# Kernel optimization log

Measured on AMD Instinct MI355X. Metric: run time of the kernel, lower is better.

## Reference

```python
import jax, jax.numpy as jnp
import numpy as np

B, L_IN, L_OUT, N, COV, EMB, H = 32, 336, 48, 512, 4, 32, 64
C = 1 + COV
D_IN = EMB + COV


def setup_inputs() -> dict:
    key = jax.random.key(0)
    ks = jax.random.split(key, 16)
    s = 1.0 / np.sqrt(H)

    def rn(k, shape, scale):
        return jax.random.normal(k, shape, jnp.float32) * scale

    return {
        "history_data": jax.random.normal(ks[0], (B, L_IN, N, C), jnp.float32),
        "future_data": jax.random.normal(ks[1], (B, L_OUT, N, C), jnp.float32),
        "emb_W": rn(ks[2], (EMB, 1), 0.5),
        "emb_b": rn(ks[3], (EMB,), 0.1),
        "W_ih0": rn(ks[4], (4 * H, D_IN), s),
        "W_hh0": rn(ks[5], (4 * H, H), s),
        "b_ih0": rn(ks[6], (4 * H,), s),
        "b_hh0": rn(ks[7], (4 * H,), s),
        "W_ih1": rn(ks[8], (4 * H, H), s),
        "W_hh1": rn(ks[9], (4 * H, H), s),
        "b_ih1": rn(ks[10], (4 * H,), s),
        "b_hh1": rn(ks[11], (4 * H,), s),
        "head_W": rn(ks[12], (2, H), s),
        "head_b": rn(ks[13], (2,), 0.1),
        "train": 1,
    }


def _lstm_cell(x_t, h, c, W_ih, W_hh, b_ih, b_hh):
    # gate order i, f, g, o (torch nn.LSTM convention)
    g = x_t @ W_ih.T + b_ih + h @ W_hh.T + b_hh
    i, f, gg, o = jnp.split(g, 4, axis=-1)
    c = jax.nn.sigmoid(f) * c + jax.nn.sigmoid(i) * jnp.tanh(gg)
    h = jax.nn.sigmoid(o) * jnp.tanh(c)
    return h, c


def _deepar_forward(history_data, future_data, emb_W, emb_b,
                    W_ih0, W_hh0, b_ih0, b_hh0,
                    W_ih1, W_hh1, b_ih1, b_hh1,
                    head_W, head_b):
    Bb, L_in, Nn, _ = history_data.shape
    L_out = future_data.shape[1]
    # [B, L_in+L_out, N, .]
    target = jnp.concatenate([history_data[..., 0:1], future_data[..., 0:1]], axis=1)
    covar = jnp.concatenate([history_data[..., 1:], future_data[..., 1:]], axis=1)
    # train=True branch: teacher forcing for t = 1 .. L-1
    prev = target[:, :-1]        # [B, T, N, 1]
    cov_t = covar[:, 1:]         # [B, T, N, COV]
    emb = prev @ emb_W.T + emb_b  # [B, T, N, EMB]
    x = jnp.concatenate([emb, cov_t], axis=-1)      # [B, T, N, EMB+COV]
    T = x.shape[1]
    x = x.transpose(1, 0, 2, 3).reshape(T, Bb * Nn, -1)  # scan over time
    Hh = W_hh0.shape[1]
    z = jnp.zeros((Bb * Nn, Hh), x.dtype)

    def step(carry, x_t):
        h0, c0, h1, c1 = carry
        h0, c0 = _lstm_cell(x_t, h0, c0, W_ih0, W_hh0, b_ih0, b_hh0)
        h1, c1 = _lstm_cell(h0, h1, c1, W_ih1, W_hh1, b_ih1, b_hh1)
        p = jax.nn.relu(h1) @ head_W.T + head_b       # [BN, 2]
        mu = p[:, 0:1]
        sigma = jax.nn.softplus(p[:, 1:2])
        return (h0, c0, h1, c1), jnp.concatenate([mu, sigma], axis=-1)

    _, outs = jax.lax.scan(step, (z, z, z, z), x)     # [T, BN, 2]
    outs = outs.reshape(T, Bb, Nn, 2).transpose(1, 0, 2, 3)  # [B, T, N, 2]
    return outs[:, -L_out:]


def reference(history_data, future_data, emb_W, emb_b,
              W_ih0, W_hh0, b_ih0, b_hh0,
              W_ih1, W_hh1, b_ih1, b_hh1,
              head_W, head_b, train):
    # train is a static Python int (1 = teacher forcing branch implemented here)
    return _deepar_forward(history_data, future_data, emb_W, emb_b,
                           W_ih0, W_hh0, b_ih0, b_hh0,
                           W_ih1, W_hh1, b_ih1, b_hh1,
                           head_W, head_b)
```

## Files before the change

kernel.cpp:

```cpp
#include <hip/hip_runtime.h>


#define T_STEPS 383
#define AST 168

typedef __attribute__((ext_vector_type(8))) short short8;
typedef __attribute__((ext_vector_type(4))) short s16x4;
typedef __attribute__((ext_vector_type(4))) float floatx4;

__device__ __forceinline__ unsigned short f2bf(float f){
  union { float f; unsigned u; } v; v.f = f;
  unsigned u = v.u + 0x7fffu + ((v.u >> 16) & 1u);
  return (unsigned short)(u >> 16);
}
__device__ __forceinline__ unsigned short f2bf_fast(float f){
  union { float f; unsigned u; } v; v.f = f;
  return (unsigned short)((v.u + 0x8000u) >> 16);
}
__device__ __forceinline__ float bf2f(unsigned short b){
  union { unsigned u; float f; } v; v.u = ((unsigned)b) << 16; return v.f;
}
__device__ __forceinline__ float fsig(float x){
  return __builtin_amdgcn_rcpf(1.f + __expf(-x));
}
__device__ __forceinline__ float ftanh(float x){
  return 1.f - 2.f * __builtin_amdgcn_rcpf(1.f + __expf(2.f * x));
}

__global__ __launch_bounds__(512, 4) void deepar_kernel(
    const float* __restrict__ hist, const float* __restrict__ fut,
    const float* __restrict__ embW, const float* __restrict__ embB,
    const float* __restrict__ Wih0, const float* __restrict__ Whh0,
    const float* __restrict__ bih0, const float* __restrict__ bhh0,
    const float* __restrict__ Wih1, const float* __restrict__ Whh1,
    const float* __restrict__ bih1, const float* __restrict__ bhh1,
    const float* __restrict__ headW, const float* __restrict__ headB,
    float* __restrict__ outp)
{
  const int tid  = threadIdx.x;
  const int lane = tid & 63;
  const int wv   = tid >> 6;
  const int l15  = lane & 15;
  const int quad = lane >> 4;
  const int koff = quad * 8;
  const int jt   = wv >> 1;
  const int mt   = wv & 1;
  const int srow = mt * 16 + l15;
  const int jbase = jt * 16 + quad * 4;

  const int b  = blockIdx.x >> 4;
  const int n0 = (blockIdx.x & 15) * 32;

  __shared__ __align__(16) unsigned short A[32 * AST];
  __shared__ __align__(16) unsigned short W1[64 * 64 * 8];
  __shared__ float HW[128];

  for (int i = tid; i < 32 * AST; i += 512) A[i] = 0;
  if (tid < 128) HW[tid] = headW[tid];
  __syncthreads();
  if (tid < 32){
    A[tid * AST + 133] = 0x3f80;
    A[tid * AST + 134] = 0x3f80;
  }
  const float hb0 = headB[0], hb1 = headB[1];

  short8 bf0[4][3];
  floatx4 bi1v[4];
  #pragma unroll
  for (int g = 0; g < 4; ++g){
    const int rf = g * 64 + jt * 16 + l15;
    float u = 0.f, bb = bih0[rf] + bhh0[rf];
    #pragma unroll
    for (int e = 0; e < 32; ++e){
      float wval = Wih0[rf * 36 + e];
      u  += wval * embW[e];
      bb += wval * embB[e];
    }
    const unsigned short bbq = f2bf(bb);
    const float bbr = bb - bf2f(bbq);
    #pragma unroll
    for (int kf = 0; kf < 2; ++kf)
      #pragma unroll
      for (int j = 0; j < 8; ++j)
        bf0[g][kf][j] = (short)f2bf(Whh0[rf * 64 + kf * 32 + koff + j]);
    #pragma unroll
    for (int j = 0; j < 8; ++j){
      const int kk = koff + j;
      float v = 0.f;
      if (kk == 0) v = u;
      else if (kk >= 1 && kk <= 4) v = Wih0[rf * 36 + 32 + (kk - 1)];
      else if (kk == 6) v = bbr;
      unsigned short q16 = (kk == 5) ? bbq : f2bf(v);
      bf0[g][2][j] = (short)q16;
    }
    #pragma unroll
    for (int q = 0; q < 4; ++q){
      const int re = g * 64 + jt * 16 + quad * 4 + q;
      bi1v[g][q] = bih1[re] + bhh1[re];
    }
    if (mt == 0){
      #pragma unroll
      for (int kf = 0; kf < 4; ++kf){
        const float* src = (kf < 2) ? (Wih1 + rf * 64 + kf * 32)
                                    : (Whh1 + rf * 64 + (kf - 2) * 32);
        short8 w;
        #pragma unroll
        for (int j = 0; j < 8; ++j)
          w[j] = (short)f2bf(src[koff + j]);
        *(short8*)&W1[((jt * 16 + g * 4 + kf) * 64 + lane) * 8] = w;
      }
    }
  }

  const bool isPrev = (tid < 32);
  const bool isCov  = (tid >= 64 && tid < 192);
  int ss = 0, cc = 0;
  if (isPrev){ ss = tid; cc = 0; }
  if (isCov) { ss = (tid - 64) >> 2; cc = 1 + ((tid - 64) & 3); }
  const int myN = n0 + ss;

  auto loadSlab = [&](int tt) -> float {
    if (isPrev){
      int l = tt; if (l > 383) l = 383;
      return (l < 336) ? hist[(((size_t)b * 336 + l) * 512 + myN) * 5]
                       : fut [(((size_t)b * 48 + (l - 336)) * 512 + myN) * 5];
    } else if (isCov){
      int l = tt + 1; if (l > 383) l = 383;
      return (l < 336) ? hist[(((size_t)b * 336 + l) * 512 + myN) * 5 + cc]
                       : fut [(((size_t)b * 48 + (l - 336)) * 512 + myN) * 5 + cc];
    }
    return 0.f;
  };

  float rIn = loadSlab(0);
  if (isPrev || isCov) A[ss * AST + 128 + cc] = f2bf(rIn);
  rIn = loadSlab(1);

  float c0s[4], c1s[4];
  #pragma unroll
  for (int i = 0; i < 4; ++i){ c0s[i] = 0.f; c1s[i] = 0.f; }

  const int xbase = srow * AST + koff;
  const int sbase = srow * AST + jbase;

  __syncthreads();

  for (int t = 0; t < T_STEPS; ++t){
    floatx4 acc[4];
    #pragma unroll
    for (int g = 0; g < 4; ++g){ floatx4 z = {0.f, 0.f, 0.f, 0.f}; acc[g] = z; }
    {
      const short8 x0 = *(const short8*)&A[xbase];
      const short8 x1 = *(const short8*)&A[xbase + 32];
      const short8 x2 = *(const short8*)&A[xbase + 128];
      #pragma unroll
      for (int g = 0; g < 4; ++g){
        acc[g] = __builtin_amdgcn_mfma_f32_16x16x32_bf16(bf0[g][0], x0, acc[g], 0, 0, 0);
        acc[g] = __builtin_amdgcn_mfma_f32_16x16x32_bf16(bf0[g][1], x1, acc[g], 0, 0, 0);
        acc[g] = __builtin_amdgcn_mfma_f32_16x16x32_bf16(bf0[g][2], x2, acc[g], 0, 0, 0);
      }
    }
    float hn[4];
    #pragma unroll
    for (int q = 0; q < 4; ++q){
      float iv = acc[0][q], fv = acc[1][q];
      float gv = acc[2][q], ov = acc[3][q];
      float c = fsig(fv) * c0s[q] + fsig(iv) * ftanh(gv);
      c0s[q] = c;
      hn[q] = fsig(ov) * ftanh(c);
    }
    __syncthreads();
    {
      s16x4 pk;
      #pragma unroll
      for (int q = 0; q < 4; ++q) pk[q] = (short)f2bf_fast(hn[q]);
      *(s16x4*)&A[sbase] = pk;
    }
    if (isPrev || isCov) A[ss * AST + 128 + cc] = f2bf_fast(rIn);
    rIn = loadSlab(t + 2);
    __syncthreads();

    #pragma unroll
    for (int g = 0; g < 4; ++g) acc[g] = bi1v[g];
    #pragma unroll
    for (int kf = 0; kf < 4; ++kf){
      const short8 xf = *(const short8*)&A[xbase + kf * 32];
      const short8 w0 = *(const short8*)&W1[((jt * 16 +  0 + kf) * 64 + lane) * 8];
      const short8 w1 = *(const short8*)&W1[((jt * 16 +  4 + kf) * 64 + lane) * 8];
      const short8 w2 = *(const short8*)&W1[((jt * 16 +  8 + kf) * 64 + lane) * 8];
      const short8 w3 = *(const short8*)&W1[((jt * 16 + 12 + kf) * 64 + lane) * 8];
      acc[0] = __builtin_amdgcn_mfma_f32_16x16x32_bf16(w0, xf, acc[0], 0, 0, 0);
      acc[1] = __builtin_amdgcn_mfma_f32_16x16x32_bf16(w1, xf, acc[1], 0, 0, 0);
      acc[2] = __builtin_amdgcn_mfma_f32_16x16x32_bf16(w2, xf, acc[2], 0, 0, 0);
      acc[3] = __builtin_amdgcn_mfma_f32_16x16x32_bf16(w3, xf, acc[3], 0, 0, 0);
    }
    #pragma unroll
    for (int q = 0; q < 4; ++q){
      float iv = acc[0][q], fv = acc[1][q];
      float gv = acc[2][q], ov = acc[3][q];
      float c = fsig(fv) * c1s[q] + fsig(iv) * ftanh(gv);
      c1s[q] = c;
      hn[q] = fsig(ov) * ftanh(c);
    }
    __syncthreads();
    {
      s16x4 pk;
      #pragma unroll
      for (int q = 0; q < 4; ++q) pk[q] = (short)f2bf_fast(hn[q]);
      *(s16x4*)&A[sbase + 64] = pk;
    }

    if (t >= 335){
      __syncthreads();
      if (tid < 256){
        const int hs = tid >> 3, outc = (tid >> 2) & 1, part = tid & 3;
        const short8 hv0 = *(const short8*)&A[hs * AST + 64 + part * 16];
        const short8 hv1 = *(const short8*)&A[hs * AST + 64 + part * 16 + 8];
        float p = 0.f;
        #pragma unroll
        for (int jj = 0; jj < 8; ++jj){
          float a0 = fmaxf(bf2f((unsigned short)hv0[jj]), 0.f);
          float a1 = fmaxf(bf2f((unsigned short)hv1[jj]), 0.f);
          p += a0 * HW[outc * 64 + part * 16 + jj];
          p += a1 * HW[outc * 64 + part * 16 + 8 + jj];
        }
        p += __shfl_xor(p, 1);
        p += __shfl_xor(p, 2);
        if ((tid & 3) == 0){
          float val;
          if (outc == 0) val = p + hb0;
          else {
            float x = p + hb1;
            val = fmaxf(x, 0.f) + __logf(1.f + __expf(-fabsf(x)));
          }
          outp[(((size_t)b * 48 + (t - 335)) * 512 + (n0 + hs)) * 2 + outc] = val;
        }
      }
    }
  }
}

extern "C" void kernel_launch(void* const* d_in, const int* in_sizes, int n_in,
                              void* d_out, int out_size, void* d_ws, size_t ws_size,
                              hipStream_t stream) {
  (void)in_sizes; (void)n_in; (void)out_size; (void)d_ws; (void)ws_size;
  deepar_kernel<<<dim3(512), dim3(512), 0, stream>>>(
      (const float*)d_in[0],  (const float*)d_in[1],
      (const float*)d_in[2],  (const float*)d_in[3],
      (const float*)d_in[4],  (const float*)d_in[5],
      (const float*)d_in[6],  (const float*)d_in[7],
      (const float*)d_in[8],  (const float*)d_in[9],
      (const float*)d_in[10], (const float*)d_in[11],
      (const float*)d_in[12], (const float*)d_in[13],
      (float*)d_out);
}
```

Measured before the change: 1.402 ms.

## Wavefront-skew LSTM layers into one phase and halve block to 256 threads

```diff
diff --git a/kernel.cpp b/kernel.cpp
--- a/kernel.cpp
+++ b/kernel.cpp
@@ -1,7 +1,7 @@
 #include <hip/hip_runtime.h>
 
 
-#define T_STEPS 383
+#define N_PHASES 385
 #define AST 168
 
 typedef __attribute__((ext_vector_type(8))) short short8;
@@ -27,7 +27,7 @@
   return 1.f - 2.f * __builtin_amdgcn_rcpf(1.f + __expf(2.f * x));
 }
 
-__global__ __launch_bounds__(512, 4) void deepar_kernel(
+__global__ __launch_bounds__(256, 2) void deepar_kernel(
     const float* __restrict__ hist, const float* __restrict__ fut,
     const float* __restrict__ embW, const float* __restrict__ embB,
     const float* __restrict__ Wih0, const float* __restrict__ Whh0,
@@ -43,9 +43,7 @@
   const int l15  = lane & 15;
   const int quad = lane >> 4;
   const int koff = quad * 8;
-  const int jt   = wv >> 1;
-  const int mt   = wv & 1;
-  const int srow = mt * 16 + l15;
+  const int jt   = wv;
   const int jbase = jt * 16 + quad * 4;
 
   const int b  = blockIdx.x >> 4;
@@ -55,7 +53,7 @@
   __shared__ __align__(16) unsigned short W1[64 * 64 * 8];
   __shared__ float HW[128];
 
-  for (int i = tid; i < 32 * AST; i += 512) A[i] = 0;
+  for (int i = tid; i < 32 * AST; i += 256) A[i] = 0;
   if (tid < 128) HW[tid] = headW[tid];
   __syncthreads();
   if (tid < 32){
@@ -98,17 +96,15 @@
       const int re = g * 64 + jt * 16 + quad * 4 + q;
       bi1v[g][q] = bih1[re] + bhh1[re];
     }
-    if (mt == 0){
-      #pragma unroll
-      for (int kf = 0; kf < 4; ++kf){
-        const float* src = (kf < 2) ? (Wih1 + rf * 64 + kf * 32)
-                                    : (Whh1 + rf * 64 + (kf - 2) * 32);
-        short8 w;
-        #pragma unroll
-        for (int j = 0; j < 8; ++j)
-          w[j] = (short)f2bf(src[koff + j]);
-        *(short8*)&W1[((jt * 16 + g * 4 + kf) * 64 + lane) * 8] = w;
-      }
+    #pragma unroll
+    for (int kf = 0; kf < 4; ++kf){
+      const float* src = (kf < 2) ? (Wih1 + rf * 64 + kf * 32)
+                                  : (Whh1 + rf * 64 + (kf - 2) * 32);
+      short8 w;
+      #pragma unroll
+      for (int j = 0; j < 8; ++j)
+        w[j] = (short)f2bf(src[koff + j]);
+      *(short8*)&W1[((jt * 16 + g * 4 + kf) * 64 + lane) * 8] = w;
     }
   }
 
@@ -136,107 +132,142 @@
   if (isPrev || isCov) A[ss * AST + 128 + cc] = f2bf(rIn);
   rIn = loadSlab(1);
 
-  float c0s[4], c1s[4];
+  float c0s[8], c1s[8];
   #pragma unroll
-  for (int i = 0; i < 4; ++i){ c0s[i] = 0.f; c1s[i] = 0.f; }
-
-  const int xbase = srow * AST + koff;
-  const int sbase = srow * AST + jbase;
+  for (int i = 0; i < 8; ++i){ c0s[i] = 0.f; c1s[i] = 0.f; }
 
   __syncthreads();
 
-  for (int t = 0; t < T_STEPS; ++t){
-    floatx4 acc[4];
-    #pragma unroll
-    for (int g = 0; g < 4; ++g){ floatx4 z = {0.f, 0.f, 0.f, 0.f}; acc[g] = z; }
-    {
-      const short8 x0 = *(const short8*)&A[xbase];
-      const short8 x1 = *(const short8*)&A[xbase + 32];
-      const short8 x2 = *(const short8*)&A[xbase + 128];
-      #pragma unroll
-      for (int g = 0; g < 4; ++g){
-        acc[g] = __builtin_amdgcn_mfma_f32_16x16x32_bf16(bf0[g][0], x0, acc[g], 0, 0, 0);
-        acc[g] = __builtin_amdgcn_mfma_f32_16x16x32_bf16(bf0[g][1], x1, acc[g], 0, 0, 0);
-        acc[g] = __builtin_amdgcn_mfma_f32_16x16x32_bf16(bf0[g][2], x2, acc[g], 0, 0, 0);
-      }
-    }
-    float hn[4];
-    #pragma unroll
-    for (int q = 0; q < 4; ++q){
-      float iv = acc[0][q], fv = acc[1][q];
-      float gv = acc[2][q], ov = acc[3][q];
-      float c = fsig(fv) * c0s[q] + fsig(iv) * ftanh(gv);
-      c0s[q] = c;
-      hn[q] = fsig(ov) * ftanh(c);
-    }
+  for (int p = 0; p < N_PHASES; ++p){
+    const bool doL0 = (p <= 382);
+    const bool doL1 = (p >= 1 && p <= 383);
+
+    short8 xh0[2][2], xh1[2][2], xin[2];
+    #pragma unroll
+    for (int mt = 0; mt < 2; ++mt){
+      const int rbase = (mt * 16 + l15) * AST;
+      xh0[mt][0] = *(const short8*)&A[rbase +  0 + koff];
+      xh0[mt][1] = *(const short8*)&A[rbase + 32 + koff];
+      xh1[mt][0] = *(const short8*)&A[rbase + 64 + koff];
+      xh1[mt][1] = *(const short8*)&A[rbase + 96 + koff];
+      xin[mt]    = *(const short8*)&A[rbase + 128 + koff];
+    }
+
+    floatx4 acc0[4][2], acc1[4][2];
+    #pragma unroll
+    for (int g = 0; g < 4; ++g)
+      #pragma unroll
+      for (int mt = 0; mt < 2; ++mt){
+        floatx4 z = {0.f, 0.f, 0.f, 0.f};
+        acc0[g][mt] = z;
+        acc1[g][mt] = bi1v[g];
+      }
+
+    if (doL0){
+      #pragma unroll
+      for (int mt = 0; mt < 2; ++mt)
+        #pragma unroll
+        for (int g = 0; g < 4; ++g){
+          acc0[g][mt] = __builtin_amdgcn_mfma_f32_16x16x32_bf16(bf0[g][0], xh0[mt][0], acc0[g][mt], 0, 0, 0);
+          acc0[g][mt] = __builtin_amdgcn_mfma_f32_16x16x32_bf16(bf0[g][1], xh0[mt][1], acc0[g][mt], 0, 0, 0);
+          acc0[g][mt] = __builtin_amdgcn_mfma_f32_16x16x32_bf16(bf0[g][2], xin[mt],   acc0[g][mt], 0, 0, 0);
+        }
+    }
+    if (doL1){
+      #pragma unroll
+      for (int kf = 0; kf < 4; ++kf){
+        const short8 w0 = *(const short8*)&W1[((jt * 16 +  0 + kf) * 64 + lane) * 8];
+        const short8 w1 = *(const short8*)&W1[((jt * 16 +  4 + kf) * 64 + lane) * 8];
+        const short8 w2 = *(const short8*)&W1[((jt * 16 +  8 + kf) * 64 + lane) * 8];
+        const short8 w3 = *(const short8*)&W1[((jt * 16 + 12 + kf) * 64 + lane) * 8];
+        #pragma unroll
+        for (int mt = 0; mt < 2; ++mt){
+          const short8 xf = (kf < 2) ? xh0[mt][kf] : xh1[mt][kf - 2];
+          acc1[0][mt] = __builtin_amdgcn_mfma_f32_16x16x32_bf16(w0, xf, acc1[0][mt], 0, 0, 0);
+          acc1[1][mt] = __builtin_amdgcn_mfma_f32_16x16x32_bf16(w1, xf, acc1[1][mt], 0, 0, 0);
+          acc1[2][mt] = __builtin_amdgcn_mfma_f32_16x16x32_bf16(w2, xf, acc1[2][mt], 0, 0, 0);
+          acc1[3][mt] = __builtin_amdgcn_mfma_f32_16x16x32_bf16(w3, xf, acc1[3][mt], 0, 0, 0);
+        }
+      }
+    }
+
+    float hn0[8], hn1[8];
+    if (doL0){
+      #pragma unroll
+      for (int mt = 0; mt < 2; ++mt)
+        #pragma unroll
+        for (int q = 0; q < 4; ++q){
+          const int idx = mt * 4 + q;
+          float iv = acc0[0][mt][q], fv = acc0[1][mt][q];
+          float gv = acc0[2][mt][q], ov = acc0[3][mt][q];
+          float c = fsig(fv) * c0s[idx] + fsig(iv) * ftanh(gv);
+          c0s[idx] = c;
+          hn0[idx] = fsig(ov) * ftanh(c);
+        }
+    }
+    if (doL1){
+      #pragma unroll
+      for (int mt = 0; mt < 2; ++mt)
+        #pragma unroll
+        for (int q = 0; q < 4; ++q){
+          const int idx = mt * 4 + q;
+          float iv = acc1[0][mt][q], fv = acc1[1][mt][q];
+          float gv = acc1[2][mt][q], ov = acc1[3][mt][q];
+          float c = fsig(fv) * c1s[idx] + fsig(iv) * ftanh(gv);
+          c1s[idx] = c;
+          hn1[idx] = fsig(ov) * ftanh(c);
+        }
+    }
+
+    if (p >= 337){
+      const int hs = tid >> 3, outc = (tid >> 2) & 1, part = tid & 3;
+      const short8 hv0 = *(const short8*)&A[hs * AST + 64 + part * 16];
+      const short8 hv1 = *(const short8*)&A[hs * AST + 64 + part * 16 + 8];
+      float pv = 0.f;
+      #pragma unroll
+      for (int jj = 0; jj < 8; ++jj){
+        float a0 = fmaxf(bf2f((unsigned short)hv0[jj]), 0.f);
+        float a1 = fmaxf(bf2f((unsigned short)hv1[jj]), 0.f);
+        pv += a0 * HW[outc * 64 + part * 16 + jj];
+        pv += a1 * HW[outc * 64 + part * 16 + 8 + jj];
+      }
+      pv += __shfl_xor(pv, 1);
+      pv += __shfl_xor(pv, 2);
+      if ((tid & 3) == 0){
+        float val;
+        if (outc == 0) val = pv + hb0;
+        else {
+          float x = pv + hb1;
+          val = fmaxf(x, 0.f) + __logf(1.f + __expf(-fabsf(x)));
+        }
+        outp[(((size_t)b * 48 + (p - 337)) * 512 + (n0 + hs)) * 2 + outc] = val;
+      }
+    }
+
     __syncthreads();
-    {
-      s16x4 pk;
-      #pragma unroll
-      for (int q = 0; q < 4; ++q) pk[q] = (short)f2bf_fast(hn[q]);
-      *(s16x4*)&A[sbase] = pk;
+
+    if (doL0){
+      #pragma unroll
+      for (int mt = 0; mt < 2; ++mt){
+        s16x4 pk;
+        #pragma unroll
+        for (int q = 0; q < 4; ++q) pk[q] = (short)f2bf_fast(hn0[mt * 4 + q]);
+        *(s16x4*)&A[(mt * 16 + l15) * AST + jbase] = pk;
+      }
+    }
+    if (doL1){
+      #pragma unroll
+      for (int mt = 0; mt < 2; ++mt){
+        s16x4 pk;
+        #pragma unroll
+        for (int q = 0; q < 4; ++q) pk[q] = (short)f2bf_fast(hn1[mt * 4 + q]);
+        *(s16x4*)&A[(mt * 16 + l15) * AST + 64 + jbase] = pk;
+      }
     }
     if (isPrev || isCov) A[ss * AST + 128 + cc] = f2bf_fast(rIn);
-    rIn = loadSlab(t + 2);
+    rIn = loadSlab(p + 2);
+
     __syncthreads();
-
-    #pragma unroll
-    for (int g = 0; g < 4; ++g) acc[g] = bi1v[g];
-    #pragma unroll
-    for (int kf = 0; kf < 4; ++kf){
-      const short8 xf = *(const short8*)&A[xbase + kf * 32];
-      const short8 w0 = *(const short8*)&W1[((jt * 16 +  0 + kf) * 64 + lane) * 8];
-      const short8 w1 = *(const short8*)&W1[((jt * 16 +  4 + kf) * 64 + lane) * 8];
-      const short8 w2 = *(const short8*)&W1[((jt * 16 +  8 + kf) * 64 + lane) * 8];
-      const short8 w3 = *(const short8*)&W1[((jt * 16 + 12 + kf) * 64 + lane) * 8];
-      acc[0] = __builtin_amdgcn_mfma_f32_16x16x32_bf16(w0, xf, acc[0], 0, 0, 0);
-      acc[1] = __builtin_amdgcn_mfma_f32_16x16x32_bf16(w1, xf, acc[1], 0, 0, 0);
-      acc[2] = __builtin_amdgcn_mfma_f32_16x16x32_bf16(w2, xf, acc[2], 0, 0, 0);
-      acc[3] = __builtin_amdgcn_mfma_f32_16x16x32_bf16(w3, xf, acc[3], 0, 0, 0);
-    }
-    #pragma unroll
-    for (int q = 0; q < 4; ++q){
-      float iv = acc[0][q], fv = acc[1][q];
-      float gv = acc[2][q], ov = acc[3][q];
-      float c = fsig(fv) * c1s[q] + fsig(iv) * ftanh(gv);
-      c1s[q] = c;
-      hn[q] = fsig(ov) * ftanh(c);
-    }
-    __syncthreads();
-    {
-      s16x4 pk;
-      #pragma unroll
-      for (int q = 0; q < 4; ++q) pk[q] = (short)f2bf_fast(hn[q]);
-      *(s16x4*)&A[sbase + 64] = pk;
-    }
-
-    if (t >= 335){
-      __syncthreads();
-      if (tid < 256){
-        const int hs = tid >> 3, outc = (tid >> 2) & 1, part = tid & 3;
-        const short8 hv0 = *(const short8*)&A[hs * AST + 64 + part * 16];
-        const short8 hv1 = *(const short8*)&A[hs * AST + 64 + part * 16 + 8];
-        float p = 0.f;
-        #pragma unroll
-        for (int jj = 0; jj < 8; ++jj){
-          float a0 = fmaxf(bf2f((unsigned short)hv0[jj]), 0.f);
-          float a1 = fmaxf(bf2f((unsigned short)hv1[jj]), 0.f);
-          p += a0 * HW[outc * 64 + part * 16 + jj];
-          p += a1 * HW[outc * 64 + part * 16 + 8 + jj];
-        }
-        p += __shfl_xor(p, 1);
-        p += __shfl_xor(p, 2);
-        if ((tid & 3) == 0){
-          float val;
-          if (outc == 0) val = p + hb0;
-          else {
-            float x = p + hb1;
-            val = fmaxf(x, 0.f) + __logf(1.f + __expf(-fabsf(x)));
-          }
-          outp[(((size_t)b * 48 + (t - 335)) * 512 + (n0 + hs)) * 2 + outc] = val;
-        }
-      }
-    }
   }
 }
 
@@ -244,7 +275,7 @@
                               void* d_out, int out_size, void* d_ws, size_t ws_size,
                               hipStream_t stream) {
   (void)in_sizes; (void)n_in; (void)out_size; (void)d_ws; (void)ws_size;
-  deepar_kernel<<<dim3(512), dim3(512), 0, stream>>>(
+  deepar_kernel<<<dim3(512), dim3(256), 0, stream>>>(
       (const float*)d_in[0],  (const float*)d_in[1],
       (const float*)d_in[2],  (const float*)d_in[3],
       (const float*)d_in[4],  (const float*)d_in[5],
```

Measured after the change: 1.455 ms. +3.7%, slower.
